# Optimization experiments

Hardware: AMD Instinct MI355X
Metric: run time of the kernel (lower is better)

The kernel has to match this reference:

```python
import jax, jax.numpy as jnp
import numpy as np

N_HEADS = 16
HEAD = 64
HID = 1024
WIN = 256
LN_EPS = 1e-5


def _ln(x, g, b):
    m = jnp.mean(x, axis=-1, keepdims=True)
    v = jnp.mean((x - m) ** 2, axis=-1, keepdims=True)
    return (x - m) * jax.lax.rsqrt(v + LN_EPS) * g + b


def _window_shift(x):
    return jnp.concatenate([jnp.zeros_like(x[:, :WIN]), x[:, :-WIN]], axis=1)


def _additive_attn(x, vec, mask_add):
    B, S, _ = x.shape
    # per-head logits: (x * vec) summed within each head, scaled
    attn = (x * vec).reshape(B, S, N_HEADS, HEAD).sum(-1) / (HEAD ** 0.5)
    attn = jnp.exp(attn + mask_add)[..., None]          # [B,S,H,1]
    xh = x.reshape(B, S, N_HEADS, HEAD)
    s = jnp.cumsum(attn * xh, axis=1)
    s = s - _window_shift(s)                             # windowed cumsum of attn*x
    z = jnp.cumsum(attn, axis=1)
    z = z - _window_shift(z)                             # windowed cumsum of attn
    return (s / z).reshape(B, S, HID)


def setup_inputs():
    key = jax.random.key(0)
    ks = jax.random.split(key, 7)
    B, S = 4, 4096
    w = lambda k: (jax.random.normal(k, (HID, HID)) * 0.02).astype(jnp.float32)
    return {
        "hidden_states": jax.random.normal(ks[0], (B, S, HID), dtype=jnp.float32),
        "attention_mask": jnp.ones((B, S), dtype=jnp.float32),
        "Wq": w(ks[1]), "Wk": w(ks[2]), "Wv": w(ks[3]), "Wp": w(ks[4]),
        "query_attn": (jax.random.normal(ks[5], (HID,)) * 0.02).astype(jnp.float32),
        "key_attn": (jax.random.normal(ks[6], (HID,)) * 0.02).astype(jnp.float32),
        "ln1_g": jnp.ones((HID,), jnp.float32), "ln1_b": jnp.zeros((HID,), jnp.float32),
        "ln2_g": jnp.ones((HID,), jnp.float32), "ln2_b": jnp.zeros((HID,), jnp.float32),
    }


def reference(hidden_states, attention_mask, Wq, Wk, Wv, Wp, query_attn, key_attn,
              ln1_g, ln1_b, ln2_g, ln2_b):
    h = _ln(hidden_states, ln1_g, ln1_b)
    query = h @ Wq.T
    keys = h @ Wk.T
    values = h @ Wv.T
    mask_add = ((1.0 - attention_mask) * -10000.0)[:, :, None]  # [B,S,1]
    pooled_q = _additive_attn(query, query_attn, mask_add)
    pooled_q = pooled_q @ Wp.T                                  # (dropout is identity in eval)
    residual = h + pooled_q * keys
    mixed = _ln(residual, ln2_g, ln2_b)
    pooled_k = _additive_attn(mixed, key_attn, mask_add)
    return residual + pooled_k * values
```

## Files before the change

kernel.cpp:

```cpp
#include <hip/hip_runtime.h>
#include <hip/hip_bf16.h>

#define HID 1024
#define NH 16
#define HEAD 64
#define WIN 256
#define SEQ 4096
#define BATCH 4
#define NROWS (BATCH * SEQ)
#define LN_EPS 1e-5f

typedef unsigned short u16;
typedef __bf16 bf16x8 __attribute__((ext_vector_type(8)));
typedef float f32x4 __attribute__((ext_vector_type(4)));

static __device__ inline float bfu(u16 u) {
    union { unsigned int i; float f; } x;
    x.i = ((unsigned int)u) << 16;
    return x.f;
}

static __device__ inline u16 f2bf(float f) {
    union { float f; unsigned int i; } x;
    x.f = f;
    unsigned int lsb = (x.i >> 16) & 1u;
    x.i += 0x7fffu + lsb;
    return (u16)(x.i >> 16);
}

__global__ __launch_bounds__(256) void ln1_conv(
    const float* __restrict__ x, const float* __restrict__ g,
    const float* __restrict__ b, u16* __restrict__ out,
    const float* __restrict__ wq, const float* __restrict__ wk,
    const float* __restrict__ wv, const float* __restrict__ wp,
    u16* __restrict__ wo)
{
    __shared__ float red[8];
    int t = threadIdx.x;
    if (blockIdx.x >= NROWS) {
        int i = (blockIdx.x - NROWS) * 256 + t;
        const int n = 1024 * 1024;
        wo[i]         = f2bf(wq[i]);
        wo[n + i]     = f2bf(wk[i]);
        wo[2 * n + i] = f2bf(wv[i]);
        wo[3 * n + i] = f2bf(wp[i]);
        return;
    }
    int row = blockIdx.x;
    float4 v = ((const float4*)(x + (size_t)row * HID))[t];
    float s  = v.x + v.y + v.z + v.w;
    float ss = v.x * v.x + v.y * v.y + v.z * v.z + v.w * v.w;
    #pragma unroll
    for (int off = 32; off; off >>= 1) { s += __shfl_down(s, off); ss += __shfl_down(ss, off); }
    int wave = t >> 6, lane = t & 63;
    if (lane == 0) { red[wave] = s; red[4 + wave] = ss; }
    __syncthreads();
    float S  = red[0] + red[1] + red[2] + red[3];
    float SS = red[4] + red[5] + red[6] + red[7];
    float mean = S * (1.f / HID);
    float var  = SS * (1.f / HID) - mean * mean;
    float inv  = rsqrtf(var + LN_EPS);
    float4 gv = ((const float4*)g)[t];
    float4 bv = ((const float4*)b)[t];
    ushort4 o;
    o.x = f2bf((v.x - mean) * inv * gv.x + bv.x);
    o.y = f2bf((v.y - mean) * inv * gv.y + bv.y);
    o.z = f2bf((v.z - mean) * inv * gv.z + bv.z);
    o.w = f2bf((v.w - mean) * inv * gv.w + bv.w);
    ((ushort4*)(out + (size_t)row * HID))[t] = o;
}

#define GLDS(gp, lp) __builtin_amdgcn_global_load_lds( \
    (const __attribute__((address_space(1))) void*)(gp), \
    (__attribute__((address_space(3))) void*)(lp), 16, 0, 0)

#define PHASE(MH, KH, LOADB, STAGE_CODE, WAIT_CODE)                            \
  {                                                                            \
    if (LOADB) {                                                               \
      _Pragma("unroll") for (int n = 0; n < 4; ++n)                            \
        bF[n] = *(const bf16x8*)&rB[wc * 4096 +                                \
            (n * 16 + (lane & 15)) * 64 + ((c0 ^ ((KH) << 6)) >> 1)];          \
    }                                                                          \
    bf16x8 aF[4];                                                              \
    _Pragma("unroll") for (int i = 0; i < 4; ++i) {                            \
      const int mf = (MH) * 4 + i;                                             \
      aF[i] = *(const bf16x8*)&rA[(mf >> 1) * 4096 +                           \
          (wr * 32 + (mf & 1) * 16 + (lane & 15)) * 64 +                       \
          ((c0 ^ ((KH) << 6)) >> 1)];                                          \
    }                                                                          \
    STAGE_CODE                                                                 \
    WAIT_CODE                                                                  \
    __builtin_amdgcn_s_barrier();                                              \
    __builtin_amdgcn_sched_barrier(0);                                         \
    __builtin_amdgcn_s_setprio(1);                                             \
    _Pragma("unroll") for (int i = 0; i < 4; ++i)                              \
      _Pragma("unroll") for (int n = 0; n < 4; ++n)                            \
        acc[(MH) * 4 + i][n] = __builtin_amdgcn_mfma_f32_16x16x32_bf16(        \
            aF[i], bF[n], acc[(MH) * 4 + i][n], 0, 0, 0);                      \
    __builtin_amdgcn_s_setprio(0);                                             \
    __builtin_amdgcn_s_barrier();                                              \
    __builtin_amdgcn_sched_barrier(0);                                         \
  }

__global__ __launch_bounds__(512, 2) void gemm256(
    const u16* __restrict__ A, const u16* __restrict__ W,
    u16* __restrict__ C, int K, int ldc, int ntiles)
{
    __shared__ __align__(16) u16 sA[2][256 * 64];
    __shared__ __align__(16) u16 sB[2][256 * 64];

    const int tid = threadIdx.x;
    const int wave = tid >> 6, lane = tid & 63;
    const int wr = wave >> 2, wc = wave & 3;

    const int rp = tid >> 3;
    const int rowA = (rp < 32 ? rp : rp + 96);
    const int colE = (((tid & 7) * 16) ^ ((rp & 7) << 4)) >> 1;
    const int c0 = ((lane >> 4) * 16) ^ ((lane & 7) << 4);

    const int nk = K >> 6;

    int a = blockIdx.x;
    int wgl = a >> 3;
    int bm = (a & 7) * 8 + (wgl & 7);
    int bn = wgl >> 3;
    const u16* gA = A + (size_t)(bm * 256 + rowA) * K + colE;
    const u16* gB = W + (size_t)(bn * 256 + rp) * K + colE;
    #pragma unroll
    for (int w = 0; w < 4; ++w) GLDS(gB + (size_t)w * 64 * K, &sB[0][w * 4096 + tid * 8]);
    #pragma unroll
    for (int p = 0; p < 4; ++p) GLDS(gA + (size_t)p * 32 * K, &sA[0][p * 4096 + tid * 8]);

    while (true) {
        asm volatile("s_waitcnt vmcnt(2)" ::: "memory");
        __builtin_amdgcn_s_barrier();
        __builtin_amdgcn_sched_barrier(0);

        f32x4 acc[8][4];
        #pragma unroll
        for (int m = 0; m < 8; ++m)
            #pragma unroll
            for (int n = 0; n < 4; ++n) {
                f32x4 z = {0.f, 0.f, 0.f, 0.f};
                acc[m][n] = z;
            }

        for (int kt = 0; kt < nk; ++kt) {
            const int b = kt & 1;
            const u16* rA = sA[b];
            const u16* rB = sB[b];
            u16* dA = sA[b ^ 1];
            u16* dB = sB[b ^ 1];
            const bool pf = (kt + 1 < nk);
            const size_t ko = (size_t)(kt + 1) * 64;
            bf16x8 bF[4];

            PHASE(0, 0, true,
                { if (pf) { GLDS(gB + ko,                      &dB[0 * 4096 + tid * 8]);
                            GLDS(gB + (size_t)1 * 64 * K + ko, &dB[1 * 4096 + tid * 8]); } },
                { if (pf) asm volatile("s_waitcnt vmcnt(2)" ::: "memory");
                  else    asm volatile("s_waitcnt vmcnt(0)" ::: "memory"); })
            PHASE(1, 0, false,
                { if (pf) { GLDS(gB + (size_t)2 * 64 * K + ko, &dB[2 * 4096 + tid * 8]);
                            GLDS(gB + (size_t)3 * 64 * K + ko, &dB[3 * 4096 + tid * 8]); } },
                { })
            PHASE(0, 1, true,
                { if (pf) { GLDS(gA + ko,                      &dA[0 * 4096 + tid * 8]);
                            GLDS(gA + (size_t)1 * 32 * K + ko, &dA[1 * 4096 + tid * 8]); } },
                { })
            PHASE(1, 1, false,
                { if (pf) { GLDS(gA + (size_t)2 * 32 * K + ko, &dA[2 * 4096 + tid * 8]);
                            GLDS(gA + (size_t)3 * 32 * K + ko, &dA[3 * 4096 + tid * 8]); } },
                { if (pf) asm volatile("s_waitcnt vmcnt(2)" ::: "memory"); })
        }

        const int bmC = bm, bnC = bn;
        a += gridDim.x;
        const bool more = (a < ntiles);
        if (more) {
            wgl = a >> 3; bm = (a & 7) * 8 + (wgl & 7); bn = wgl >> 3;
            gA = A + (size_t)(bm * 256 + rowA) * K + colE;
            gB = W + (size_t)(bn * 256 + rp) * K + colE;
            #pragma unroll
            for (int w = 0; w < 4; ++w) GLDS(gB + (size_t)w * 64 * K, &sB[0][w * 4096 + tid * 8]);
            #pragma unroll
            for (int p = 0; p < 4; ++p) GLDS(gA + (size_t)p * 32 * K, &sA[0][p * 4096 + tid * 8]);
        }

        #pragma unroll
        for (int mf = 0; mf < 8; ++mf) {
            int row0 = bmC * 256 + wr * 128 + mf * 16 + ((lane >> 4) << 2);
            #pragma unroll
            for (int n = 0; n < 4; ++n) {
                int col = bnC * 256 + wc * 64 + n * 16 + (lane & 15);
                #pragma unroll
                for (int r = 0; r < 4; ++r)
                    C[(size_t)(row0 + r) * ldc + col] = f2bf(acc[mf][n][r]);
            }
        }
        if (!more) break;
    }
}

__global__ __launch_bounds__(256) void logits_kernel(
    const u16* __restrict__ x, int xstride,
    const float* __restrict__ vec, const float* __restrict__ mask,
    float* __restrict__ aw)
{
    int h = blockIdx.y, b = blockIdx.z;
    int s = blockIdx.x * 256 + threadIdx.x;
    __shared__ float vl[HEAD];
    if (threadIdx.x < HEAD) vl[threadIdx.x] = vec[h * HEAD + threadIdx.x];
    __syncthreads();
    const uint4* xr = (const uint4*)(x + ((size_t)(b * SEQ + s)) * xstride + h * HEAD);
    float dot = 0.f;
    #pragma unroll
    for (int i = 0; i < 8; ++i) {
        uint4 v = xr[i];
        const u16* p = (const u16*)&v;
        #pragma unroll
        for (int j = 0; j < 8; ++j) dot += bfu(p[j]) * vl[i * 8 + j];
    }
    float ma = (1.0f - mask[b * SEQ + s]) * -10000.0f;
    aw[((size_t)b * NH + h) * SEQ + s] = expf(dot * 0.125f + ma);
}

__global__ __launch_bounds__(512) void attn_win2(
    const u16* __restrict__ x, int xstride,
    const float* __restrict__ aw_g,
    u16* __restrict__ out_bf,
    const u16* __restrict__ resv,
    float* __restrict__ outF,
    int fused)
{
    int c = blockIdx.x, h2 = blockIdx.y, b = blockIdx.z;
    __shared__ float awl[2][2][WIN];
    __shared__ float2 sts[2][8][64];
    __shared__ float stz[2][8][2];

    int t = threadIdx.x, wave = t >> 6, lane = t & 63;
    int hh = lane >> 5;
    int coff = hh * 64 + (lane & 31) * 2;
    bool havePrev = (c > 0);

    const float* aw0 = aw_g + ((size_t)b * NH + h2 * 2) * SEQ;
    for (int i = t; i < 1024; i += 512) {
        int hd = i >> 9, cc = (i >> 8) & 1, j = i & 255;
        float v = 0.f;
        if (cc == 1) v = aw0[hd * SEQ + c * WIN + j];
        else if (havePrev) v = aw0[hd * SEQ + (c - 1) * WIN + j];
        awl[hd][cc][j] = v;
    }
    __syncthreads();

    const u16* xb = x + (size_t)b * SEQ * xstride + h2 * 128 + coff;
    int jp0 = (havePrev ? c - 1 : c) * WIN;
    int jc0 = c * WIN;
    int j0 = wave * 32;

    float s0a = 0, s0b = 0, s1a = 0, s1b = 0, z0 = 0, z1 = 0;
    #pragma unroll 8
    for (int jj = 0; jj < 32; ++jj) {
        int j = j0 + jj;
        float ap = awl[hh][0][j], ac = awl[hh][1][j];
        unsigned up = *(const unsigned*)(xb + (size_t)(jp0 + j) * xstride);
        unsigned uc = *(const unsigned*)(xb + (size_t)(jc0 + j) * xstride);
        s0a += ap * bfu(up & 0xffff); s0b += ap * bfu(up >> 16); z0 += ap;
        s1a += ac * bfu(uc & 0xffff); s1b += ac * bfu(uc >> 16); z1 += ac;
    }
    sts[0][wave][lane] = make_float2(s0a, s0b);
    sts[1][wave][lane] = make_float2(s1a, s1b);
    if ((lane & 31) == 0) { stz[0][wave][hh] = z0; stz[1][wave][hh] = z1; }
    __syncthreads();

    float cs0a = 0, cs0b = 0, cs1a = 0, cs1b = 0, cz0 = 0, cz1 = 0;
    float totsa = 0, totsb = 0, totz = 0;
    #pragma unroll
    for (int w2 = 0; w2 < 8; ++w2) {
        float2 sp = sts[0][w2][lane];
        float zp = stz[0][w2][hh];
        totsa += sp.x; totsb += sp.y; totz += zp;
        if (w2 < wave) {
            cs0a += sp.x; cs0b += sp.y; cz0 += zp;
            float2 sc = sts[1][w2][lane];
            cs1a += sc.x; cs1b += sc.y; cz1 += stz[1][w2][hh];
        }
    }

    float rpa = cs0a, rpb = cs0b, rca = cs1a, rcb = cs1b, rzp = cz0, rzc = cz1;
    size_t rowbase = (size_t)b * SEQ + jc0;
    #pragma unroll 4
    for (int jj = 0; jj < 32; ++jj) {
        int j = j0 + jj;
        float ap = awl[hh][0][j], ac = awl[hh][1][j];
        unsigned up = *(const unsigned*)(xb + (size_t)(jp0 + j) * xstride);
        unsigned uc = *(const unsigned*)(xb + (size_t)(jc0 + j) * xstride);
        rpa += ap * bfu(up & 0xffff); rpb += ap * bfu(up >> 16); rzp += ap;
        rca += ac * bfu(uc & 0xffff); rcb += ac * bfu(uc >> 16); rzc += ac;
        float inv = 1.f / (rzc + totz - rzp);
        float wva = (rca + totsa - rpa) * inv;
        float wvb = (rcb + totsb - rpb) * inv;
        if (fused) {
            size_t roff = (rowbase + j) * 3072 + h2 * 128 + coff;
            unsigned rr = *(const unsigned*)(resv + roff);
            unsigned vv = *(const unsigned*)(resv + roff + 2048);
            float2 o;
            o.x = bfu(rr & 0xffff) + wva * bfu(vv & 0xffff);
            o.y = bfu(rr >> 16)    + wvb * bfu(vv >> 16);
            *(float2*)(outF + (rowbase + j) * HID + h2 * 128 + coff) = o;
        } else {
            unsigned pk = (unsigned)f2bf(wva) | ((unsigned)f2bf(wvb) << 16);
            *(unsigned*)(out_bf + (rowbase + j) * HID + h2 * 128 + coff) = pk;
        }
    }
}

__global__ __launch_bounds__(256) void resid_ln2(
    const u16* h, u16* qkv,
    const float* __restrict__ g, const float* __restrict__ b,
    const float* __restrict__ ka, const float* __restrict__ mask,
    u16* mixed, float* __restrict__ aw2)
{
    int row = blockIdx.x;
    int t = threadIdx.x;
    ushort4 h4 = ((const ushort4*)(h + (size_t)row * HID))[t];
    ushort4 p4 = ((const ushort4*)(qkv + (size_t)row * 3072))[t];
    ushort4 k4 = ((const ushort4*)(qkv + (size_t)row * 3072 + 1024))[t];
    float r0 = bfu(h4.x) + bfu(p4.x) * bfu(k4.x);
    float r1 = bfu(h4.y) + bfu(p4.y) * bfu(k4.y);
    float r2 = bfu(h4.z) + bfu(p4.z) * bfu(k4.z);
    float r3 = bfu(h4.w) + bfu(p4.w) * bfu(k4.w);
    ushort4 rb;
    rb.x = f2bf(r0); rb.y = f2bf(r1); rb.z = f2bf(r2); rb.w = f2bf(r3);
    ((ushort4*)(qkv + (size_t)row * 3072))[t] = rb;

    float s  = r0 + r1 + r2 + r3;
    float ss = r0 * r0 + r1 * r1 + r2 * r2 + r3 * r3;
    __shared__ float red[8];
    #pragma unroll
    for (int off = 32; off; off >>= 1) { s += __shfl_down(s, off); ss += __shfl_down(ss, off); }
    int wave = t >> 6, lane = t & 63;
    if (lane == 0) { red[wave] = s; red[4 + wave] = ss; }
    __syncthreads();
    float S  = red[0] + red[1] + red[2] + red[3];
    float SS = red[4] + red[5] + red[6] + red[7];
    float mean = S * (1.f / HID);
    float var  = SS * (1.f / HID) - mean * mean;
    float inv  = rsqrtf(var + LN_EPS);
    float4 gv = ((const float4*)g)[t];
    float4 bv = ((const float4*)b)[t];
    float n0 = (r0 - mean) * inv * gv.x + bv.x;
    float n1 = (r1 - mean) * inv * gv.y + bv.y;
    float n2 = (r2 - mean) * inv * gv.z + bv.z;
    float n3 = (r3 - mean) * inv * gv.w + bv.w;
    ushort4 o;
    o.x = f2bf(n0); o.y = f2bf(n1); o.z = f2bf(n2); o.w = f2bf(n3);
    ((ushort4*)(mixed + (size_t)row * HID))[t] = o;

    float4 kv = ((const float4*)ka)[t];
    float partial = n0 * kv.x + n1 * kv.y + n2 * kv.z + n3 * kv.w;
    partial += __shfl_xor(partial, 1);
    partial += __shfl_xor(partial, 2);
    partial += __shfl_xor(partial, 4);
    partial += __shfl_xor(partial, 8);
    if ((t & 15) == 0) {
        int hh = t >> 4;
        int bb = row >> 12, sl = row & (SEQ - 1);
        float ma = (1.0f - mask[row]) * -10000.0f;
        aw2[((size_t)bb * NH + hh) * SEQ + sl] = expf(partial * 0.125f + ma);
    }
}

extern "C" void kernel_launch(void* const* d_in, const int* in_sizes, int n_in,
                              void* d_out, int out_size, void* d_ws, size_t ws_size,
                              hipStream_t stream)
{
    const float* hidden = (const float*)d_in[0];
    const float* mask   = (const float*)d_in[1];
    const float* Wq     = (const float*)d_in[2];
    const float* Wk     = (const float*)d_in[3];
    const float* Wv     = (const float*)d_in[4];
    const float* Wp     = (const float*)d_in[5];
    const float* qa     = (const float*)d_in[6];
    const float* ka     = (const float*)d_in[7];
    const float* g1     = (const float*)d_in[8];
    const float* b1     = (const float*)d_in[9];
    const float* g2     = (const float*)d_in[10];
    const float* b2     = (const float*)d_in[11];
    float* out = (float*)d_out;

    char* ws = (char*)d_ws;
    u16* wbf = (u16*)ws;       ws += (size_t)4 * 1024 * 1024 * 2;
    u16* hbf = (u16*)ws;       ws += (size_t)NROWS * HID * 2;
    u16* qkv = (u16*)ws;       ws += (size_t)NROWS * 3072 * 2;
    u16* pooled = (u16*)ws;    ws += (size_t)NROWS * HID * 2;
    float* aw1 = (float*)ws;   ws += (size_t)BATCH * NH * SEQ * 4;
    float* aw2 = (float*)ws;

    ln1_conv<<<NROWS + 4096, 256, 0, stream>>>(hidden, g1, b1, hbf, Wq, Wk, Wv, Wp, wbf);
    gemm256<<<256, 512, 0, stream>>>(hbf, wbf, qkv, HID, 3072, 768);
    logits_kernel<<<dim3(SEQ / 256, NH, BATCH), 256, 0, stream>>>(qkv, 3072, qa, mask, aw1);
    attn_win2<<<dim3(SEQ / WIN, NH / 2, BATCH), 512, 0, stream>>>(
        qkv, 3072, aw1, pooled, (const u16*)nullptr, (float*)nullptr, 0);
    gemm256<<<256, 512, 0, stream>>>(pooled, wbf + (size_t)3 * 1024 * 1024, qkv, HID, 3072, 256);
    resid_ln2<<<NROWS, 256, 0, stream>>>(hbf, qkv, g2, b2, ka, mask, hbf, aw2);
    attn_win2<<<dim3(SEQ / WIN, NH / 2, BATCH), 512, 0, stream>>>(
        hbf, HID, aw2, (u16*)nullptr, qkv, out, 1);
}
```

Baseline: 274.7 us.

## Replace four-phase interleaved GEMM pipeline with single-stage prefetch per k-tile

Drops the PHASE macro, which split each 64-wide k-tile into four sub-phases, each with its own barriers and staggered global-to-LDS loads. Each k-iteration now issues all eight next-tile loads up front and waits for the current buffer with vmcnt(8). It then loads all A/B fragments for both k-halves and runs 64 MFMAs between just two barriers. This aims to cut barrier and scheduling overhead, at the cost of coarser overlap between loads and math. It also raises register pressure, since 16 A fragments and 8 B fragments are live alongside 128 accumulator registers, so spills are a risk.

```diff
diff --git a/kernel.cpp b/kernel.cpp
--- a/kernel.cpp
+++ b/kernel.cpp
@@ -74,34 +74,6 @@
     (const __attribute__((address_space(1))) void*)(gp), \
     (__attribute__((address_space(3))) void*)(lp), 16, 0, 0)
 
-#define PHASE(MH, KH, LOADB, STAGE_CODE, WAIT_CODE)                            \
-  {                                                                            \
-    if (LOADB) {                                                               \
-      _Pragma("unroll") for (int n = 0; n < 4; ++n)                            \
-        bF[n] = *(const bf16x8*)&rB[wc * 4096 +                                \
-            (n * 16 + (lane & 15)) * 64 + ((c0 ^ ((KH) << 6)) >> 1)];          \
-    }                                                                          \
-    bf16x8 aF[4];                                                              \
-    _Pragma("unroll") for (int i = 0; i < 4; ++i) {                            \
-      const int mf = (MH) * 4 + i;                                             \
-      aF[i] = *(const bf16x8*)&rA[(mf >> 1) * 4096 +                           \
-          (wr * 32 + (mf & 1) * 16 + (lane & 15)) * 64 +                       \
-          ((c0 ^ ((KH) << 6)) >> 1)];                                          \
-    }                                                                          \
-    STAGE_CODE                                                                 \
-    WAIT_CODE                                                                  \
-    __builtin_amdgcn_s_barrier();                                              \
-    __builtin_amdgcn_sched_barrier(0);                                         \
-    __builtin_amdgcn_s_setprio(1);                                             \
-    _Pragma("unroll") for (int i = 0; i < 4; ++i)                              \
-      _Pragma("unroll") for (int n = 0; n < 4; ++n)                            \
-        acc[(MH) * 4 + i][n] = __builtin_amdgcn_mfma_f32_16x16x32_bf16(        \
-            aF[i], bF[n], acc[(MH) * 4 + i][n], 0, 0, 0);                      \
-    __builtin_amdgcn_s_setprio(0);                                             \
-    __builtin_amdgcn_s_barrier();                                              \
-    __builtin_amdgcn_sched_barrier(0);                                         \
-  }
-
 __global__ __launch_bounds__(512, 2) void gemm256(
     const u16* __restrict__ A, const u16* __restrict__ W,
     u16* __restrict__ C, int K, int ldc, int ntiles)
@@ -117,6 +89,7 @@
     const int rowA = (rp < 32 ? rp : rp + 96);
     const int colE = (((tid & 7) * 16) ^ ((rp & 7) << 4)) >> 1;
     const int c0 = ((lane >> 4) * 16) ^ ((lane & 7) << 4);
+    const int li = lane & 15;
 
     const int nk = K >> 6;
 
@@ -132,10 +105,6 @@
     for (int p = 0; p < 4; ++p) GLDS(gA + (size_t)p * 32 * K, &sA[0][p * 4096 + tid * 8]);
 
     while (true) {
-        asm volatile("s_waitcnt vmcnt(2)" ::: "memory");
-        __builtin_amdgcn_s_barrier();
-        __builtin_amdgcn_sched_barrier(0);
-
         f32x4 acc[8][4];
         #pragma unroll
         for (int m = 0; m < 8; ++m)
@@ -152,26 +121,55 @@
             u16* dA = sA[b ^ 1];
             u16* dB = sB[b ^ 1];
             const bool pf = (kt + 1 < nk);
-            const size_t ko = (size_t)(kt + 1) * 64;
-            bf16x8 bF[4];
-
-            PHASE(0, 0, true,
-                { if (pf) { GLDS(gB + ko,                      &dB[0 * 4096 + tid * 8]);
-                            GLDS(gB + (size_t)1 * 64 * K + ko, &dB[1 * 4096 + tid * 8]); } },
-                { if (pf) asm volatile("s_waitcnt vmcnt(2)" ::: "memory");
-                  else    asm volatile("s_waitcnt vmcnt(0)" ::: "memory"); })
-            PHASE(1, 0, false,
-                { if (pf) { GLDS(gB + (size_t)2 * 64 * K + ko, &dB[2 * 4096 + tid * 8]);
-                            GLDS(gB + (size_t)3 * 64 * K + ko, &dB[3 * 4096 + tid * 8]); } },
-                { })
-            PHASE(0, 1, true,
-                { if (pf) { GLDS(gA + ko,                      &dA[0 * 4096 + tid * 8]);
-                            GLDS(gA + (size_t)1 * 32 * K + ko, &dA[1 * 4096 + tid * 8]); } },
-                { })
-            PHASE(1, 1, false,
-                { if (pf) { GLDS(gA + (size_t)2 * 32 * K + ko, &dA[2 * 4096 + tid * 8]);
-                            GLDS(gA + (size_t)3 * 32 * K + ko, &dA[3 * 4096 + tid * 8]); } },
-                { if (pf) asm volatile("s_waitcnt vmcnt(2)" ::: "memory"); })
+
+            if (pf) {
+                const size_t ko = (size_t)(kt + 1) * 64;
+                #pragma unroll
+                for (int w = 0; w < 4; ++w)
+                    GLDS(gB + (size_t)w * 64 * K + ko, &dB[w * 4096 + tid * 8]);
+                #pragma unroll
+                for (int p = 0; p < 4; ++p)
+                    GLDS(gA + (size_t)p * 32 * K + ko, &dA[p * 4096 + tid * 8]);
+                asm volatile("s_waitcnt vmcnt(8)" ::: "memory");
+            } else {
+                asm volatile("s_waitcnt vmcnt(0)" ::: "memory");
+            }
+            __builtin_amdgcn_sched_barrier(0);
+            __builtin_amdgcn_s_barrier();
+            __builtin_amdgcn_sched_barrier(0);
+
+            bf16x8 bF0[4], bF1[4], aF0[8], aF1[8];
+            #pragma unroll
+            for (int n = 0; n < 4; ++n)
+                bF0[n] = *(const bf16x8*)&rB[wc * 4096 + (n * 16 + li) * 64 + (c0 >> 1)];
+            #pragma unroll
+            for (int mf = 0; mf < 8; ++mf)
+                aF0[mf] = *(const bf16x8*)&rA[(mf >> 1) * 4096 +
+                    (wr * 32 + (mf & 1) * 16 + li) * 64 + (c0 >> 1)];
+            __builtin_amdgcn_s_setprio(1);
+            #pragma unroll
+            for (int mf = 0; mf < 8; ++mf)
+                #pragma unroll
+                for (int n = 0; n < 4; ++n)
+                    acc[mf][n] = __builtin_amdgcn_mfma_f32_16x16x32_bf16(
+                        aF0[mf], bF0[n], acc[mf][n], 0, 0, 0);
+            #pragma unroll
+            for (int n = 0; n < 4; ++n)
+                bF1[n] = *(const bf16x8*)&rB[wc * 4096 + (n * 16 + li) * 64 + ((c0 ^ 64) >> 1)];
+            #pragma unroll
+            for (int mf = 0; mf < 8; ++mf)
+                aF1[mf] = *(const bf16x8*)&rA[(mf >> 1) * 4096 +
+                    (wr * 32 + (mf & 1) * 16 + li) * 64 + ((c0 ^ 64) >> 1)];
+            #pragma unroll
+            for (int mf = 0; mf < 8; ++mf)
+                #pragma unroll
+                for (int n = 0; n < 4; ++n)
+                    acc[mf][n] = __builtin_amdgcn_mfma_f32_16x16x32_bf16(
+                        aF1[mf], bF1[n], acc[mf][n], 0, 0, 0);
+            __builtin_amdgcn_s_setprio(0);
+            __builtin_amdgcn_sched_barrier(0);
+            __builtin_amdgcn_s_barrier();
+            __builtin_amdgcn_sched_barrier(0);
         }
 
         const int bmC = bm, bnC = bn;
@@ -192,7 +190,7 @@
             int row0 = bmC * 256 + wr * 128 + mf * 16 + ((lane >> 4) << 2);
             #pragma unroll
             for (int n = 0; n < 4; ++n) {
-                int col = bnC * 256 + wc * 64 + n * 16 + (lane & 15);
+                int col = bnC * 256 + wc * 64 + n * 16 + li;
                 #pragma unroll
                 for (int r = 0; r < 4; ++r)
                     C[(size_t)(row0 + r) * ldc + col] = f2bf(acc[mf][n][r]);
```

After: 283.9 us. 3.4% more time.
